# Optimization experiments

Hardware: AMD Instinct MI355X
Metric: run time of the kernel (lower is better)

## Reference

```python
import jax, jax.numpy as jnp
import numpy as np

K_ORDER = 4
BETA = 0.5
NUM_HEADS = 1
IN_CHANNELS = 128


def _gcn_conv(x, row, col, values, N):
    # x: [N, H, D]; symmetric-normalized scatter-add message passing
    deg = jax.ops.segment_sum(values, row, num_segments=N)            # [N]
    dinv = jnp.where(deg > 0, deg ** -0.5, jnp.zeros_like(deg))
    coef = dinv[row] * dinv[col] * values                             # [E]
    return jax.ops.segment_sum(x[col] * coef[:, None, None], row, num_segments=N)


def _fast_attn_conv(qs, ks, vs, batch, pos, n_nodes_f, B, max_node):
    # qs/ks/vs: [N, H, D]; ragged graphs padded to [B, max_node, H, D]
    N, H, D = vs.shape
    q_pad = jnp.zeros((B, max_node, H, D), qs.dtype).at[batch, pos].set(qs)
    k_pad = jnp.zeros((B, max_node, H, D), ks.dtype).at[batch, pos].set(ks)
    v_pad = jnp.zeros((B, max_node, H, D), vs.dtype).at[batch, pos].set(vs)
    qk = jnp.einsum('bmhd,bnhd->bmhn', q_pad, k_pad)                  # [B, M, H, M]
    v_sum = jax.ops.segment_sum(vs, batch, num_segments=B)            # [B, H, D]
    numer_pad = jnp.einsum('bmhn,bnhd->bmhd', qk, v_pad)              # [B, M, H, D]
    numer = numer_pad[batch, pos] + v_sum[batch]                      # [N, H, D]
    denom = qk[batch, pos].sum(-1) + n_nodes_f[batch][:, None]        # [N, H]
    return numer / denom[..., None]


def _forward(x, edge_weight, Wq_w, Wq_b, Wk_w, Wk_b, Wo_w, Wo_b,
             row, col, batch, pos, n_nodes_f, B, max_node):
    N, C = x.shape
    H = NUM_HEADS
    query = (x @ Wq_w.T + Wq_b).reshape(N, H, C)
    key = (x @ Wk_w.T + Wk_b).reshape(N, H, C)
    qs = query / jnp.linalg.norm(query, axis=2, keepdims=True)
    ks = key / jnp.linalg.norm(key, axis=2, keepdims=True)
    cur = jnp.broadcast_to(x[:, None, :], (N, H, C))                  # x_0
    acc = cur
    for _ in range(K_ORDER):
        gcn_i = _gcn_conv(cur, row, col, edge_weight, N)
        attn_i = _fast_attn_conv(qs, ks, cur, batch, pos, n_nodes_f, B, max_node)
        cur = BETA * gcn_i + (1.0 - BETA) * attn_i
        acc = acc + cur
    out = acc.reshape(N, H * C) @ Wo_w.T + Wo_b
    return out / H


def setup_inputs():
    key = jax.random.key(0)
    k = jax.random.split(key, 10)
    B, per_graph = 64, 512
    N = B * per_graph
    C, H, OUT = IN_CHANNELS, NUM_HEADS, 128
    E = N * 16
    s = 1.0 / np.sqrt(C)
    return {
        'x': jax.random.normal(k[0], (N, C), jnp.float32),
        'edge_index': jax.random.randint(k[1], (2, E), 0, N, jnp.int32),
        'edge_weight': jax.random.uniform(k[2], (E,), jnp.float32),
        'n_nodes': jnp.full((B,), per_graph, jnp.int32),
        'Wq_w': jax.random.uniform(k[3], (H * C, C), jnp.float32, -s, s),
        'Wq_b': jax.random.uniform(k[4], (H * C,), jnp.float32, -s, s),
        'Wk_w': jax.random.uniform(k[5], (H * C, C), jnp.float32, -s, s),
        'Wk_b': jax.random.uniform(k[6], (H * C,), jnp.float32, -s, s),
        'Wo_w': jax.random.uniform(k[7], (OUT, H * C), jnp.float32, -s, s),
        'Wo_b': jax.random.uniform(k[8], (OUT,), jnp.float32, -s, s),
    }


def reference(x, edge_index, edge_weight, n_nodes, Wq_w, Wq_b, Wk_w, Wk_b, Wo_w, Wo_b):
    n_np = np.asarray(n_nodes)
    B, max_node = n_np.shape[0], int(n_np.max())
    N = x.shape[0]
    batch = jnp.asarray(np.repeat(np.arange(B), n_np))                # [N] graph id per node
    offsets = jnp.asarray(np.concatenate([[0], np.cumsum(n_np)[:-1]]))
    pos = jnp.arange(N) - offsets[batch]                              # within-graph index
    n_nodes_f = jnp.asarray(n_np, jnp.float32)
    row, col = edge_index[0], edge_index[1]
    return _forward(x, edge_weight, Wq_w, Wq_b, Wk_w, Wk_b, Wo_w, Wo_b,
                    row, col, batch, pos, n_nodes_f, B, max_node)
```

## Files before the change

### kernel.cpp

```cpp
#include <hip/hip_runtime.h>
#include <stdint.h>

#define C 128

typedef __attribute__((ext_vector_type(8))) short bfrag;
typedef __attribute__((ext_vector_type(4))) float ffrag;

__device__ __forceinline__ unsigned short f2bf(float f){
  union { float f; unsigned int i; } v; v.f = f;
  unsigned int x = v.i;
  unsigned int r = x + 0x7fffu + ((x >> 16) & 1u);
  return (unsigned short)(r >> 16);
}
__device__ __forceinline__ float bf2f(unsigned short u){
  union { unsigned int i; float f; } v; v.i = ((unsigned int)u) << 16; return v.f;
}

__global__ void k_zero_region(unsigned int* base, int nwords){
  int i = blockIdx.x * 256 + threadIdx.x;
  if (i < nwords) base[i] = 0u;
}

__global__ __launch_bounds__(256) void k_prep1(
    const int* __restrict__ row, const float* __restrict__ w,
    unsigned long long* deg64, int* __restrict__ rank, int E, int degB,
    const float* __restrict__ x, unsigned short* __restrict__ cur0,
    unsigned short* __restrict__ curT, int N, int prepB,
    const float* __restrict__ Wq, const float* __restrict__ Wk,
    const float* __restrict__ Wo, unsigned short* __restrict__ W16, int WW){
  __shared__ unsigned short tile[64][66];
  int bx = blockIdx.x;
  if (bx < degB){
    int e = bx * 256 + threadIdx.x;
    if (e < E){
      int r = row[e];
      unsigned int wf = (unsigned int)(w[e] * 16777216.0f + 0.5f);
      unsigned long long old =
          atomicAdd(&deg64[r], 0x100000000ULL | (unsigned long long)wf);
      rank[e] = (int)(old >> 32);
    }
    return;
  }
  bx -= degB;
  if (bx < prepB){
    int ntiles = N >> 6;
    int n0 = (bx % ntiles) * 64;
    int c0 = (bx / ntiles) * 64;
    int tx = threadIdx.x & 63, ty = threadIdx.x >> 6;
    for (int r = ty; r < 64; r += 4){
      float v = x[(size_t)(n0 + r) * C + c0 + tx];
      unsigned short u = f2bf(v);
      cur0[(size_t)(n0 + r) * C + c0 + tx] = u;
      tile[r][tx] = u;
    }
    __syncthreads();
    for (int r = ty; r < 64; r += 4)
      curT[(size_t)(c0 + r) * N + n0 + tx] = tile[tx][r];
    return;
  }
  bx -= prepB;
  int i = bx * 256 + threadIdx.x;
  if (i < 3 * WW){
    const float* src = (i < WW) ? Wq : ((i < 2 * WW) ? Wk : Wo);
    int off = (i < WW) ? 0 : ((i < 2 * WW) ? WW : 2 * WW);
    W16[i] = f2bf(src[i - off]);
  }
}

__global__ void k_scan1(const unsigned long long* __restrict__ deg64,
                        float* __restrict__ dinv, int* bsum, int N){
  __shared__ int s[256];
  int b = blockIdx.x, t = threadIdx.x;
  int i = b * 256 + t;
  int cnt = 0;
  if (i < N){
    unsigned long long v = deg64[i];
    cnt = (int)(v >> 32);
    unsigned int lo = (unsigned int)v;
    float d = (float)lo * (1.0f / 16777216.0f);
    dinv[i] = lo > 0u ? 1.0f / sqrtf(d) : 0.f;
  }
  s[t] = cnt;
  __syncthreads();
  for (int o = 128; o; o >>= 1){ if (t < o) s[t] += s[t + o]; __syncthreads(); }
  if (t == 0) bsum[b] = s[0];
}

__global__ void k_scan3(const unsigned long long* __restrict__ deg64,
                        const int* __restrict__ bsum, int* row_ptr, int N){
  __shared__ int s[256];
  int b = blockIdx.x, t = threadIdx.x;
  int i = b * 256 + t;
  int v = (i < N) ? (int)(deg64[i] >> 32) : 0;
  s[t] = v;
  __syncthreads();
  for (int o = 1; o < 256; o <<= 1){
    int u = (t >= o) ? s[t - o] : 0;
    __syncthreads(); s[t] += u; __syncthreads();
  }
  int base = 0;
  for (int j = 0; j < b; j++) base += bsum[j];
  int excl = base + s[t] - v;
  if (i < N) row_ptr[i] = excl;
  if (i == N - 1) row_ptr[N] = excl + v;
}

__global__ __launch_bounds__(256) void k_prep2(
    const int* __restrict__ row, const int* __restrict__ col,
    const float* __restrict__ w, const int* __restrict__ rank,
    const int* __restrict__ row_ptr, const float* __restrict__ dinv,
    int2* __restrict__ edge_s, int E, int fillB,
    const unsigned short* __restrict__ x, const unsigned short* __restrict__ W16,
    const float* __restrict__ Wq_b, const float* __restrict__ Wk_b,
    unsigned short* __restrict__ qs, unsigned short* __restrict__ ksT,
    int N, int wblocks){
  int bx = blockIdx.x;
  if (bx < fillB){
    int e = bx * 256 + threadIdx.x;
    if (e < E){
      int r = row[e], c = col[e];
      int p = row_ptr[r] + rank[e];
      float cf = dinv[r] * dinv[c] * w[e];
      int2 ed; ed.x = c; ed.y = __float_as_int(cf);
      edge_s[p] = ed;
    }
    return;
  }
  bx -= fillB;
  int transposed = bx >= wblocks;
  int lb = transposed ? bx - wblocks : bx;
  const unsigned short* W = transposed ? (W16 + C * C) : W16;
  const float* Wb = transposed ? Wk_b : Wq_b;
  unsigned short* out = transposed ? ksT : qs;

  int wv = threadIdx.x >> 6, l = threadIdx.x & 63;
  int m0 = (lb * 4 + wv) * 16;
  if (m0 >= N) return;
  int quad = l >> 4, lcol = l & 15;
  ffrag acc[8] = {};
  const unsigned short* Abase = x + (size_t)(m0 + lcol) * C + quad * 8;
#pragma unroll
  for (int s = 0; s < 4; s++){
    bfrag a = *(const bfrag*)(Abase + s * 32);
#pragma unroll
    for (int nt = 0; nt < 8; nt++){
      bfrag bb = *(const bfrag*)(W + (size_t)(nt * 16 + lcol) * C + s * 32 + quad * 8);
      acc[nt] = __builtin_amdgcn_mfma_f32_16x16x32_bf16(a, bb, acc[nt], 0, 0, 0);
    }
  }
  float q[8][4];
  float ss[4] = {0.f, 0.f, 0.f, 0.f};
#pragma unroll
  for (int nt = 0; nt < 8; nt++){
    float bias = Wb[nt * 16 + lcol];
#pragma unroll
    for (int r = 0; r < 4; r++){ float v = acc[nt][r] + bias; q[nt][r] = v; ss[r] += v * v; }
  }
#pragma unroll
  for (int off = 1; off < 16; off <<= 1){
#pragma unroll
    for (int r = 0; r < 4; r++) ss[r] += __shfl_xor(ss[r], off, 64);
  }
  float inv[4];
#pragma unroll
  for (int r = 0; r < 4; r++) inv[r] = 1.0f / sqrtf(fmaxf(ss[r], 1e-30f));
  if (!transposed){
#pragma unroll
    for (int nt = 0; nt < 8; nt++)
#pragma unroll
      for (int r = 0; r < 4; r++)
        out[(size_t)(m0 + quad * 4 + r) * C + nt * 16 + lcol] = f2bf(q[nt][r] * inv[r]);
  } else {
#pragma unroll
    for (int nt = 0; nt < 8; nt++){
      ushort4 pk;
      pk.x = f2bf(q[nt][0] * inv[0]); pk.y = f2bf(q[nt][1] * inv[1]);
      pk.z = f2bf(q[nt][2] * inv[2]); pk.w = f2bf(q[nt][3] * inv[3]);
      *(ushort4*)(out + (size_t)(nt * 16 + lcol) * N + m0 + quad * 4) = pk;
    }
  }
}

__global__ __launch_bounds__(256) void k_mid(const unsigned short* __restrict__ ksT,
      const unsigned short* __restrict__ curT, unsigned short* __restrict__ MT,
      const int* __restrict__ row_ptr, const int2* __restrict__ edge_s,
      const unsigned int* __restrict__ cur32, unsigned int* __restrict__ gcn32,
      float* __restrict__ vsum, float* __restrict__ ksum,
      int N, int PG, int mB, int vsB, int ksB, int gcnB){
  int bx = blockIdx.x;
  if (bx < mB){
    int wv = threadIdx.x >> 6, l = threadIdx.x & 63;
    int b = bx >> 2;
    int gw = (bx & 3) * 4 + wv;
    int itile = gw & 7, jh = gw >> 3;
    int quad = l >> 4, lcol = l & 15;
    ffrag acc[4] = {};
    const unsigned short* Arow = ksT + (size_t)(itile * 16 + lcol) * N + (size_t)b * PG + quad * 8;
    const unsigned short* B0 = curT + (size_t)b * PG + quad * 8;
    int steps = PG / 32;
    for (int s = 0; s < steps; s++){
      bfrag a = *(const bfrag*)(Arow + s * 32);
#pragma unroll
      for (int jt = 0; jt < 4; jt++){
        bfrag bb = *(const bfrag*)(B0 + (size_t)((jh * 4 + jt) * 16 + lcol) * N + s * 32);
        acc[jt] = __builtin_amdgcn_mfma_f32_16x16x32_bf16(a, bb, acc[jt], 0, 0, 0);
      }
    }
    unsigned short* MTb = MT + (size_t)b * C * C;
    int i0 = itile * 16 + quad * 4;
#pragma unroll
    for (int jt = 0; jt < 4; jt++){
      int j = (jh * 4 + jt) * 16 + lcol;
      ushort4 pk;
      pk.x = f2bf(acc[jt][0]); pk.y = f2bf(acc[jt][1]);
      pk.z = f2bf(acc[jt][2]); pk.w = f2bf(acc[jt][3]);
      *(ushort4*)(MTb + (size_t)j * C + i0) = pk;
    }
    return;
  }
  bx -= mB;
  if (bx < vsB + ksB){
    const unsigned short* src = (bx < vsB) ? curT : ksT;
    float* dst = (bx < vsB) ? vsum : ksum;
    int b = (bx < vsB) ? bx : (bx - vsB);
    int wv = threadIdx.x >> 6, l = threadIdx.x & 63;
    for (int d = wv * 32; d < wv * 32 + 32; d++){
      float s = 0.f;
      for (int n0 = l * 8; n0 < PG; n0 += 512){
        bfrag v = *(const bfrag*)(src + (size_t)d * N + (size_t)b * PG + n0);
#pragma unroll
        for (int j = 0; j < 8; j++) s += bf2f((unsigned short)v[j]);
      }
#pragma unroll
      for (int off = 32; off; off >>= 1) s += __shfl_xor(s, off, 64);
      if (l == 0) dst[b * C + d] = s;
    }
    return;
  }
  bx -= vsB + ksB;
  if (bx < gcnB){
    int nid = bx * 4 + (threadIdx.x >> 6);
    int c = threadIdx.x & 63;
    if (nid >= N) return;
    int s = row_ptr[nid], e = row_ptr[nid + 1];
    float a0 = 0.f, a1 = 0.f;
    int p = s;
    for (; p + 4 <= e; p += 4){
      int2 e0 = edge_s[p],     e1 = edge_s[p + 1];
      int2 e2 = edge_s[p + 2], e3 = edge_s[p + 3];
      float f0 = __int_as_float(e0.y), f1 = __int_as_float(e1.y);
      float f2 = __int_as_float(e2.y), f3 = __int_as_float(e3.y);
      unsigned int u0 = cur32[(size_t)e0.x * 64 + c];
      unsigned int u1 = cur32[(size_t)e1.x * 64 + c];
      unsigned int u2 = cur32[(size_t)e2.x * 64 + c];
      unsigned int u3 = cur32[(size_t)e3.x * 64 + c];
      a0 += f0 * bf2f((unsigned short)(u0 & 0xffffu));
      a1 += f0 * bf2f((unsigned short)(u0 >> 16));
      a0 += f1 * bf2f((unsigned short)(u1 & 0xffffu));
      a1 += f1 * bf2f((unsigned short)(u1 >> 16));
      a0 += f2 * bf2f((unsigned short)(u2 & 0xffffu));
      a1 += f2 * bf2f((unsigned short)(u2 >> 16));
      a0 += f3 * bf2f((unsigned short)(u3 & 0xffffu));
      a1 += f3 * bf2f((unsigned short)(u3 >> 16));
    }
    for (; p < e; p++){
      int2 ed = edge_s[p];
      float cf = __int_as_float(ed.y);
      unsigned int u = cur32[(size_t)ed.x * 64 + c];
      a0 += cf * bf2f((unsigned short)(u & 0xffffu));
      a1 += cf * bf2f((unsigned short)(u >> 16));
    }
    gcn32[(size_t)nid * 64 + c] = ((unsigned int)f2bf(a1) << 16) | (unsigned int)f2bf(a0);
  }
}

__global__ __launch_bounds__(256) void k_phase2(const unsigned short* __restrict__ qs,
      const unsigned short* __restrict__ MT, const float* __restrict__ vsum,
      const float* __restrict__ ksum, const int* __restrict__ n_nodes,
      float* __restrict__ denom, const unsigned short* __restrict__ gcn16,
      unsigned short* __restrict__ curO, unsigned short* __restrict__ curT,
      int N, int PG, int it0){
  int wv = threadIdx.x >> 6, l = threadIdx.x & 63;
  int m0 = (blockIdx.x * 4 + wv) * 16;
  if (m0 >= N) return;
  int b = m0 / PG;
  int quad = l >> 4, lcol = l & 15;
  ffrag acc[8] = {};
  const unsigned short* Abase = qs + (size_t)(m0 + lcol) * C + quad * 8;
  const unsigned short* MTb = MT + (size_t)b * C * C;
  const float* ksb = ksum + b * C;
  float dsum = 0.f;
#pragma unroll
  for (int s = 0; s < 4; s++){
    bfrag a = *(const bfrag*)(Abase + s * 32);
    if (it0){
#pragma unroll
      for (int j = 0; j < 8; j++)
        dsum += bf2f((unsigned short)a[j]) * ksb[quad * 8 + s * 32 + j];
    }
#pragma unroll
    for (int dt = 0; dt < 8; dt++){
      bfrag bb = *(const bfrag*)(MTb + (size_t)(dt * 16 + lcol) * C + s * 32 + quad * 8);
      acc[dt] = __builtin_amdgcn_mfma_f32_16x16x32_bf16(a, bb, acc[dt], 0, 0, 0);
    }
  }
  float dn[4];
  if (it0){
    dsum += __shfl_xor(dsum, 16, 64);
    dsum += __shfl_xor(dsum, 32, 64);
    float dfull = dsum + (float)n_nodes[b];
    if (quad == 0) denom[m0 + lcol] = dfull;
#pragma unroll
    for (int r = 0; r < 4; r++) dn[r] = __shfl(dfull, quad * 4 + r, 64);
  } else {
#pragma unroll
    for (int r = 0; r < 4; r++) dn[r] = denom[m0 + quad * 4 + r];
  }
#pragma unroll
  for (int dt = 0; dt < 8; dt++){
    int d = dt * 16 + lcol;
    float vs = vsum[b * C + d];
    ushort4 pk;
#pragma unroll
    for (int r = 0; r < 4; r++){
      int m = m0 + quad * 4 + r;
      float attn = (acc[dt][r] + vs) / dn[r];
      float g = bf2f(gcn16[(size_t)m * C + d]);
      unsigned short nb = f2bf(0.5f * (g + attn));
      curO[(size_t)m * C + d] = nb;
      ((unsigned short*)&pk)[r] = nb;
    }
    *(ushort4*)(curT + (size_t)d * N + m0 + quad * 4) = pk;
  }
}

__global__ __launch_bounds__(256) void k_final(const float* __restrict__ x,
      const unsigned short* __restrict__ c1, const unsigned short* __restrict__ c2,
      const unsigned short* __restrict__ c3, const unsigned short* __restrict__ c4,
      const unsigned short* __restrict__ Wo, const float* __restrict__ Wob,
      float* __restrict__ out, int N){
  int wv = threadIdx.x >> 6, l = threadIdx.x & 63;
  int m0 = (blockIdx.x * 4 + wv) * 16;
  if (m0 >= N) return;
  int quad = l >> 4, lcol = l & 15;
  ffrag acc[8] = {};
  size_t rowoff = (size_t)(m0 + lcol) * C + quad * 8;
#pragma unroll
  for (int s = 0; s < 4; s++){
    size_t base = rowoff + s * 32;
    float4 xa0 = *(const float4*)(x + base);
    float4 xa1 = *(const float4*)(x + base + 4);
    bfrag b1 = *(const bfrag*)(c1 + base);
    bfrag b2 = *(const bfrag*)(c2 + base);
    bfrag b3 = *(const bfrag*)(c3 + base);
    bfrag b4 = *(const bfrag*)(c4 + base);
    float xs[8] = {xa0.x, xa0.y, xa0.z, xa0.w, xa1.x, xa1.y, xa1.z, xa1.w};
    bfrag a;
#pragma unroll
    for (int j = 0; j < 8; j++){
      float v = (((xs[j] + bf2f((unsigned short)b1[j])) + bf2f((unsigned short)b2[j]))
                 + bf2f((unsigned short)b3[j])) + bf2f((unsigned short)b4[j]);
      a[j] = (short)f2bf(v);
    }
#pragma unroll
    for (int ot = 0; ot < 8; ot++){
      bfrag bb = *(const bfrag*)(Wo + (size_t)(ot * 16 + lcol) * C + s * 32 + quad * 8);
      acc[ot] = __builtin_amdgcn_mfma_f32_16x16x32_bf16(a, bb, acc[ot], 0, 0, 0);
    }
  }
#pragma unroll
  for (int ot = 0; ot < 8; ot++){
    float bias = Wob[ot * 16 + lcol];
#pragma unroll
    for (int r = 0; r < 4; r++){
      out[(size_t)(m0 + quad * 4 + r) * C + ot * 16 + lcol] = acc[ot][r] + bias;
    }
  }
}


extern "C" void kernel_launch(void* const* d_in, const int* in_sizes, int n_in,
                              void* d_out, int out_size, void* d_ws, size_t ws_size,
                              hipStream_t stream){
  const float* x    = (const float*)d_in[0];
  const int*   eidx = (const int*)d_in[1];
  const float* ew   = (const float*)d_in[2];
  const int*   n_nodes = (const int*)d_in[3];
  const float* Wq_w = (const float*)d_in[4];
  const float* Wq_b = (const float*)d_in[5];
  const float* Wk_w = (const float*)d_in[6];
  const float* Wk_b = (const float*)d_in[7];
  const float* Wo_w = (const float*)d_in[8];
  const float* Wo_b = (const float*)d_in[9];
  float* out = (float*)d_out;

  int N = in_sizes[0] / C;
  int E = in_sizes[2];
  int B = in_sizes[3];
  int PG = N / B;
  int BC = B * C;
  const int* row = eidx;
  const int* col = eidx + E;

  char* p = (char*)d_ws;
  auto alloc = [&](size_t bytes) -> void* {
    void* r = (void*)p; p += (bytes + 255) & ~(size_t)255; return r;
  };
  unsigned short* cur[5];
  for (int i = 0; i < 5; i++) cur[i] = (unsigned short*)alloc((size_t)N * C * 2);
  unsigned short* curT  = (unsigned short*)alloc((size_t)N * C * 2);
  unsigned short* qs16  = (unsigned short*)alloc((size_t)N * C * 2);
  unsigned short* ksT   = (unsigned short*)alloc((size_t)N * C * 2);
  unsigned short* gcn16 = (unsigned short*)alloc((size_t)N * C * 2);
  unsigned short* MT    = (unsigned short*)alloc((size_t)B * C * C * 2);
  unsigned short* W16   = (unsigned short*)alloc((size_t)3 * C * C * 2);
  unsigned long long* deg64 = (unsigned long long*)alloc((size_t)N * 8);
  float*          dinv  = (float*)alloc((size_t)N * 4);
  int*            row_ptr = (int*)alloc((size_t)(N + 1) * 4);
  int*            rank  = (int*)alloc((size_t)E * 4);
  int*            bsum  = (int*)alloc(1024);
  int2*           edge_s = (int2*)alloc((size_t)E * 8);
  float*          ksum  = (float*)alloc((size_t)BC * 4);
  float*          vsum  = (float*)alloc((size_t)BC * 4);
  float*          denom = (float*)alloc((size_t)N * 4);

  dim3 b256(256);
  int wblocks = (N / 16 + 3) / 4;
  int WW = C * C;
  int nscan = (N + 255) / 256;
  int degB = (E + 255) / 256;
  int castB = (3 * WW + 255) / 256;
  int fillB = (E + 255) / 256;
  int prepB = (N / 64) * (C / 64);
  int mB = 4 * B;
  int gcnB = (N + 3) / 4;
  int vsB = B;

  k_zero_region<<<dim3((2 * N + 255) / 256), b256, 0, stream>>>((unsigned int*)deg64, 2 * N);
  k_prep1<<<dim3(degB + prepB + castB), b256, 0, stream>>>(row, ew, deg64, rank, E, degB,
                                                           x, cur[0], curT, N, prepB,
                                                           Wq_w, Wk_w, Wo_w, W16, WW);
  k_scan1<<<dim3(nscan), b256, 0, stream>>>(deg64, dinv, bsum, N);
  k_scan3<<<dim3(nscan), b256, 0, stream>>>(deg64, bsum, row_ptr, N);
  k_prep2<<<dim3(fillB + 2 * wblocks), b256, 0, stream>>>(row, col, ew, rank, row_ptr, dinv,
                                                          edge_s, E, fillB,
                                                          cur[0], W16, Wq_b, Wk_b,
                                                          qs16, ksT, N, wblocks);

  for (int it = 0; it < 4; it++){
    int ksB = (it == 0) ? B : 0;
    k_mid<<<dim3(mB + vsB + ksB + gcnB), b256, 0, stream>>>(ksT, curT, MT, row_ptr, edge_s,
                                                      (const unsigned int*)cur[it],
                                                      (unsigned int*)gcn16,
                                                      vsum, ksum,
                                                      N, PG, mB, vsB, ksB, gcnB);
    k_phase2<<<dim3(wblocks), b256, 0, stream>>>(qs16, MT, vsum, ksum, n_nodes, denom,
                                                 gcn16, cur[it + 1], curT,
                                                 N, PG, (it == 0) ? 1 : 0);
  }

  k_final<<<dim3(wblocks), b256, 0, stream>>>(x, cur[1], cur[2], cur[3], cur[4],
                                              W16 + 2 * WW, Wo_b, out, N);
}
```

Baseline: 381.8 us.

## Fuse GCN neighbor gather into phase2 via shared-memory staging

```diff
diff --git a/kernel.cpp b/kernel.cpp
--- a/kernel.cpp
+++ b/kernel.cpp
@@ -181,12 +181,10 @@
   }
 }
 
-__global__ __launch_bounds__(256) void k_mid(const unsigned short* __restrict__ ksT,
+__global__ __launch_bounds__(256) void k_M(const unsigned short* __restrict__ ksT,
       const unsigned short* __restrict__ curT, unsigned short* __restrict__ MT,
-      const int* __restrict__ row_ptr, const int2* __restrict__ edge_s,
-      const unsigned int* __restrict__ cur32, unsigned int* __restrict__ gcn32,
       float* __restrict__ vsum, float* __restrict__ ksum,
-      int N, int PG, int mB, int vsB, int ksB, int gcnB){
+      int N, int PG, int mB, int vsB, int ksB){
   int bx = blockIdx.x;
   if (bx < mB){
     int wv = threadIdx.x >> 6, l = threadIdx.x & 63;
@@ -235,13 +233,23 @@
       for (int off = 32; off; off >>= 1) s += __shfl_xor(s, off, 64);
       if (l == 0) dst[b * C + d] = s;
     }
-    return;
-  }
-  bx -= vsB + ksB;
-  if (bx < gcnB){
-    int nid = bx * 4 + (threadIdx.x >> 6);
-    int c = threadIdx.x & 63;
-    if (nid >= N) return;
+  }
+}
+
+__global__ __launch_bounds__(256) void k_phase2(const unsigned short* __restrict__ qs,
+      const unsigned short* __restrict__ MT, const float* __restrict__ vsum,
+      const float* __restrict__ ksum, const int* __restrict__ n_nodes,
+      float* __restrict__ denom,
+      const int* __restrict__ row_ptr, const int2* __restrict__ edge_s,
+      const unsigned int* __restrict__ cur32,
+      unsigned short* __restrict__ curO, unsigned short* __restrict__ curT,
+      int N, int PG, int it0){
+  __shared__ unsigned int gbuf[4][16][66];
+  int wv = threadIdx.x >> 6, l = threadIdx.x & 63;
+  int m0 = (blockIdx.x * 4 + wv) * 16;
+  if (m0 >= N) return;
+  for (int r16 = 0; r16 < 16; r16++){
+    int nid = m0 + r16;
     int s = row_ptr[nid], e = row_ptr[nid + 1];
     float a0 = 0.f, a1 = 0.f;
     int p = s;
@@ -250,10 +258,10 @@
       int2 e2 = edge_s[p + 2], e3 = edge_s[p + 3];
       float f0 = __int_as_float(e0.y), f1 = __int_as_float(e1.y);
       float f2 = __int_as_float(e2.y), f3 = __int_as_float(e3.y);
-      unsigned int u0 = cur32[(size_t)e0.x * 64 + c];
-      unsigned int u1 = cur32[(size_t)e1.x * 64 + c];
-      unsigned int u2 = cur32[(size_t)e2.x * 64 + c];
-      unsigned int u3 = cur32[(size_t)e3.x * 64 + c];
+      unsigned int u0 = cur32[(size_t)e0.x * 64 + l];
+      unsigned int u1 = cur32[(size_t)e1.x * 64 + l];
+      unsigned int u2 = cur32[(size_t)e2.x * 64 + l];
+      unsigned int u3 = cur32[(size_t)e3.x * 64 + l];
       a0 += f0 * bf2f((unsigned short)(u0 & 0xffffu));
       a1 += f0 * bf2f((unsigned short)(u0 >> 16));
       a0 += f1 * bf2f((unsigned short)(u1 & 0xffffu));
@@ -266,23 +274,12 @@
     for (; p < e; p++){
       int2 ed = edge_s[p];
       float cf = __int_as_float(ed.y);
-      unsigned int u = cur32[(size_t)ed.x * 64 + c];
+      unsigned int u = cur32[(size_t)ed.x * 64 + l];
       a0 += cf * bf2f((unsigned short)(u & 0xffffu));
       a1 += cf * bf2f((unsigned short)(u >> 16));
     }
-    gcn32[(size_t)nid * 64 + c] = ((unsigned int)f2bf(a1) << 16) | (unsigned int)f2bf(a0);
-  }
-}
-
-__global__ __launch_bounds__(256) void k_phase2(const unsigned short* __restrict__ qs,
-      const unsigned short* __restrict__ MT, const float* __restrict__ vsum,
-      const float* __restrict__ ksum, const int* __restrict__ n_nodes,
-      float* __restrict__ denom, const unsigned short* __restrict__ gcn16,
-      unsigned short* __restrict__ curO, unsigned short* __restrict__ curT,
-      int N, int PG, int it0){
-  int wv = threadIdx.x >> 6, l = threadIdx.x & 63;
-  int m0 = (blockIdx.x * 4 + wv) * 16;
-  if (m0 >= N) return;
+    gbuf[wv][r16][l] = ((unsigned int)f2bf(a1) << 16) | (unsigned int)f2bf(a0);
+  }
   int b = m0 / PG;
   int quad = l >> 4, lcol = l & 15;
   ffrag acc[8] = {};
@@ -325,7 +322,9 @@
     for (int r = 0; r < 4; r++){
       int m = m0 + quad * 4 + r;
       float attn = (acc[dt][r] + vs) / dn[r];
-      float g = bf2f(gcn16[(size_t)m * C + d]);
+      unsigned int gw = gbuf[wv][quad * 4 + r][dt * 8 + (lcol >> 1)];
+      float g = bf2f((lcol & 1) ? (unsigned short)(gw >> 16)
+                                : (unsigned short)(gw & 0xffffu));
       unsigned short nb = f2bf(0.5f * (g + attn));
       curO[(size_t)m * C + d] = nb;
       ((unsigned short*)&pk)[r] = nb;
@@ -411,7 +410,6 @@
   unsigned short* curT  = (unsigned short*)alloc((size_t)N * C * 2);
   unsigned short* qs16  = (unsigned short*)alloc((size_t)N * C * 2);
   unsigned short* ksT   = (unsigned short*)alloc((size_t)N * C * 2);
-  unsigned short* gcn16 = (unsigned short*)alloc((size_t)N * C * 2);
   unsigned short* MT    = (unsigned short*)alloc((size_t)B * C * C * 2);
   unsigned short* W16   = (unsigned short*)alloc((size_t)3 * C * C * 2);
   unsigned long long* deg64 = (unsigned long long*)alloc((size_t)N * 8);
@@ -433,7 +431,6 @@
   int fillB = (E + 255) / 256;
   int prepB = (N / 64) * (C / 64);
   int mB = 4 * B;
-  int gcnB = (N + 3) / 4;
   int vsB = B;
 
   k_zero_region<<<dim3((2 * N + 255) / 256), b256, 0, stream>>>((unsigned int*)deg64, 2 * N);
@@ -449,13 +446,12 @@
 
   for (int it = 0; it < 4; it++){
     int ksB = (it == 0) ? B : 0;
-    k_mid<<<dim3(mB + vsB + ksB + gcnB), b256, 0, stream>>>(ksT, curT, MT, row_ptr, edge_s,
-                                                      (const unsigned int*)cur[it],
-                                                      (unsigned int*)gcn16,
-                                                      vsum, ksum,
-                                                      N, PG, mB, vsB, ksB, gcnB);
+    k_M<<<dim3(mB + vsB + ksB), b256, 0, stream>>>(ksT, curT, MT, vsum, ksum,
+                                                   N, PG, mB, vsB, ksB);
     k_phase2<<<dim3(wblocks), b256, 0, stream>>>(qs16, MT, vsum, ksum, n_nodes, denom,
-                                                 gcn16, cur[it + 1], curT,
+                                                 row_ptr, edge_s,
+                                                 (const unsigned int*)cur[it],
+                                                 cur[it + 1], curT,
                                                  N, PG, (it == 0) ? 1 : 0);
   }
 
```

Result: slower. 537.4 us (+40.7%).
